# Performance work log

Hardware: AMD Instinct MI355X
Metric: run time of the kernel (lower is better)

## Reference

```python
import jax, jax.numpy as jnp
import numpy as np

ALPHA = 1.0
HALF_LOG_2PI = 0.5 * float(np.log(2.0 * np.pi))


def setup_inputs() -> dict:
    key = jax.random.key(0)
    k1, k2 = jax.random.split(key)
    N = 1024
    G = 32  # grid_size per axis
    pitch = 0.04
    # Filtered 3D points (camera-0 frame), roughly inside the crop volume.
    half_extent = G * pitch / 2.0  # 0.64 m
    points = jax.random.normal(k1, (N, 3), dtype=jnp.float32) * (half_extent / 2.0)
    # Normalized confidences after the >2.5 threshold; keep strictly positive.
    confs = jax.random.uniform(k2, (N,), dtype=jnp.float32) + 0.5
    # Voxel-center coordinates, grid centered at origin: [X, Y, Z, 3]
    lin = (jnp.arange(G, dtype=jnp.float32) - (G - 1) / 2.0) * pitch
    cx, cy, cz = jnp.meshgrid(lin, lin, lin, indexing='ij')
    coordinates = jnp.stack([cx, cy, cz], axis=-1)
    return {
        'points': points,
        'confs': confs,
        'coordinates': coordinates,
        'pitch': jnp.array([pitch], dtype=jnp.float32),
    }


def reference(points, confs, coordinates, pitch):
    # points: [N,3]; confs: [N]; coordinates: [X,Y,Z,3]; pitch: [1]
    # z = (c - p) / (alpha * conf * pitch), broadcast to [N,X,Y,Z,3]
    scale = ALPHA * confs[:, None, None, None, None] * pitch[0]  # [N,1,1,1,1]
    z = (coordinates[None] - points[:, None, None, None, :]) / scale
    # Normal(0,1).log_prob(z) = -z^2/2 - log(sqrt(2*pi))
    log_probs = -0.5 * z * z - HALF_LOG_2PI
    return log_probs
```

## Files before the change

### kernel.cpp

```cpp
#include <hip/hip_runtime.h>
#include <math.h>


#define HALF_LOG_2PI 0.91893853320467274178f

__global__ __launch_bounds__(256) void pbt_kernel(
    const float* __restrict__ points,
    const float* __restrict__ confs,
    const float* __restrict__ pitch_p,
    float* __restrict__ out)
{
    const unsigned block = blockIdx.x;
    const unsigned n = block >> 5;
    const unsigned x = block & 31u;

    const float pitch = pitch_p[0];
    const float conf  = confs[n];
    const float inv   = 1.0f / (conf * pitch);
    const float s     = pitch * inv;
    const float off   = 15.5f * pitch;
    const float bx = (off + points[n * 3 + 0]) * inv;
    const float by = (off + points[n * 3 + 1]) * inv;
    const float bz = (off + points[n * 3 + 2]) * inv;

    const float tx = (float)x * s - bx;
    const float vx = fmaf(-0.5f * tx, tx, -HALF_LOG_2PI);

    float4* o = (float4*)(out + (size_t)block * 3072u);
    const unsigned t = threadIdx.x;

    #pragma unroll
    for (int k = 0; k < 3; ++k) {
        const unsigned f4 = t + (unsigned)k * 256u;
        const unsigned e0 = f4 * 4u;
        float v[4];
        #pragma unroll
        for (int j = 0; j < 4; ++j) {
            const unsigned e  = e0 + (unsigned)j;
            const unsigned d  = e % 3u;
            const unsigned zi = e / 3u;
            const unsigned y  = zi >> 5;
            const unsigned zz = zi & 31u;
            const float ty = (float)y  * s - by;
            const float tz = (float)zz * s - bz;
            const float vy = fmaf(-0.5f * ty, ty, -HALF_LOG_2PI);
            const float vz = fmaf(-0.5f * tz, tz, -HALF_LOG_2PI);
            v[j] = (d == 0u) ? vx : ((d == 1u) ? vy : vz);
        }
        o[f4] = make_float4(v[0], v[1], v[2], v[3]);
    }
}

extern "C" void kernel_launch(void* const* d_in, const int* in_sizes, int n_in,
                              void* d_out, int out_size, void* d_ws, size_t ws_size,
                              hipStream_t stream) {
    const float* points = (const float*)d_in[0];
    const float* confs  = (const float*)d_in[1];
    const float* pitch  = (const float*)d_in[3];
    float* out = (float*)d_out;

    const int N = in_sizes[0] / 3;
    const int blocks = N * 32;
    pbt_kernel<<<dim3(blocks), dim3(256), 0, stream>>>(points, confs, pitch, out);
}
```

Before: 77.87 us.

## Process all x-slices per block, precompute y/z terms, use nontemporal stores

Each block now handles one point across all 32 x-slices instead of one slice. The per-element y/z log-prob values and x-selection masks are computed once and reused across the x loop, so each output element costs a single fma. Stores switch to nontemporal vector stores to avoid polluting cache on this write-bound kernel. Using 1024 blocks instead of 32768 cuts scheduling overhead but gives fewer blocks for latency hiding and uses more registers per thread.

After: 85.10 us. 9.3% more time.

```diff
diff --git a/kernel.cpp b/kernel.cpp
--- a/kernel.cpp
+++ b/kernel.cpp
@@ -3,6 +3,8 @@
 
 
 #define HALF_LOG_2PI 0.91893853320467274178f
+
+typedef float f32x4 __attribute__((ext_vector_type(4)));
 
 __global__ __launch_bounds__(256) void pbt_kernel(
     const float* __restrict__ points,
@@ -10,9 +12,8 @@
     const float* __restrict__ pitch_p,
     float* __restrict__ out)
 {
-    const unsigned block = blockIdx.x;
-    const unsigned n = block >> 5;
-    const unsigned x = block & 31u;
+    const unsigned n = blockIdx.x;
+    const unsigned t = threadIdx.x;
 
     const float pitch = pitch_p[0];
     const float conf  = confs[n];
@@ -23,17 +24,11 @@
     const float by = (off + points[n * 3 + 1]) * inv;
     const float bz = (off + points[n * 3 + 2]) * inv;
 
-    const float tx = (float)x * s - bx;
-    const float vx = fmaf(-0.5f * tx, tx, -HALF_LOG_2PI);
-
-    float4* o = (float4*)(out + (size_t)block * 3072u);
-    const unsigned t = threadIdx.x;
-
+    float vbase[3][4];
+    float isx[3][4];
     #pragma unroll
     for (int k = 0; k < 3; ++k) {
-        const unsigned f4 = t + (unsigned)k * 256u;
-        const unsigned e0 = f4 * 4u;
-        float v[4];
+        const unsigned e0 = (t + (unsigned)k * 256u) * 4u;
         #pragma unroll
         for (int j = 0; j < 4; ++j) {
             const unsigned e  = e0 + (unsigned)j;
@@ -41,13 +36,30 @@
             const unsigned zi = e / 3u;
             const unsigned y  = zi >> 5;
             const unsigned zz = zi & 31u;
-            const float ty = (float)y  * s - by;
-            const float tz = (float)zz * s - bz;
-            const float vy = fmaf(-0.5f * ty, ty, -HALF_LOG_2PI);
-            const float vz = fmaf(-0.5f * tz, tz, -HALF_LOG_2PI);
-            v[j] = (d == 0u) ? vx : ((d == 1u) ? vy : vz);
+            const float c  = (d == 2u) ? (float)zz : (float)y;
+            const float b  = (d == 2u) ? bz : by;
+            const float tc = c * s - b;
+            const float v  = fmaf(-0.5f * tc, tc, -HALF_LOG_2PI);
+            isx[k][j]   = (d == 0u) ? 1.0f : 0.0f;
+            vbase[k][j] = (d == 0u) ? 0.0f : v;
         }
-        o[f4] = make_float4(v[0], v[1], v[2], v[3]);
+    }
+
+    f32x4* o = (f32x4*)(out + (size_t)n * 98304u) + t;
+    #pragma unroll 2
+    for (unsigned x = 0; x < 32u; ++x) {
+        const float tx = (float)x * s - bx;
+        const float vx = fmaf(-0.5f * tx, tx, -HALF_LOG_2PI);
+        f32x4* ox = o + (size_t)x * 768u;
+        #pragma unroll
+        for (int k = 0; k < 3; ++k) {
+            f32x4 v;
+            v.x = fmaf(isx[k][0], vx, vbase[k][0]);
+            v.y = fmaf(isx[k][1], vx, vbase[k][1]);
+            v.z = fmaf(isx[k][2], vx, vbase[k][2]);
+            v.w = fmaf(isx[k][3], vx, vbase[k][3]);
+            __builtin_nontemporal_store(v, ox + k * 256);
+        }
     }
 }
 
@@ -60,6 +72,5 @@
     float* out = (float*)d_out;
 
     const int N = in_sizes[0] / 3;
-    const int blocks = N * 32;
-    pbt_kernel<<<dim3(blocks), dim3(256), 0, stream>>>(points, confs, pitch, out);
+    pbt_kernel<<<dim3(N), dim3(256), 0, stream>>>(points, confs, pitch, out);
 }
```
